# Optimization experiments

Hardware: AMD Instinct MI355X
Metric: run time of the kernel (lower is better)

The kernel has to match this reference:

```python
import jax, jax.numpy as jnp
import numpy as np

D = 1024      # n_embd
F = 1024      # moe_inter_dim (ffn_hidden_size)
E = 8         # moe_num_experts
K = 2         # moe_top_k
B, T = 2, 2048


def setup_inputs() -> dict:
    key = jax.random.key(0)
    ks = jax.random.split(key, 7)
    std = 0.02
    x = jax.random.normal(ks[0], (B, T, D), dtype=jnp.float32)
    router_w = jax.random.normal(ks[1], (D, E), dtype=jnp.float32) * std
    w1 = jax.random.normal(ks[2], (E, D, F), dtype=jnp.float32) * std  # expert up proj
    w2 = jax.random.normal(ks[3], (E, F, D), dtype=jnp.float32) * std  # expert down proj
    shared_gate_up = jax.random.normal(ks[4], (D, 2 * F), dtype=jnp.float32) * std
    shared_down = jax.random.normal(ks[5], (F, D), dtype=jnp.float32) * std
    shared_gate_w = jax.random.normal(ks[6], (D, 1), dtype=jnp.float32) * std
    return {"x": x, "router_w": router_w, "w1": w1, "w2": w2,
            "shared_gate_up": shared_gate_up, "shared_down": shared_down,
            "shared_gate_w": shared_gate_w}


def _moe_forward(x, router_w, w1, w2, shared_gate_up, shared_down, shared_gate_w):
    b, t, d = x.shape
    xf = x.reshape(-1, d)                                   # [N, D]
    n = xf.shape[0]

    # --- router: softmax over experts, top-k scores used directly as combine weights ---
    logits = xf @ router_w                                  # [N, E]
    probs = jax.nn.softmax(logits, axis=-1)
    topw, topi = jax.lax.top_k(probs, K)                    # [N, K]
    combine = jnp.zeros((n, E), dtype=probs.dtype).at[
        jnp.arange(n)[:, None], topi].add(topw)             # [N, E] sparse combine weights

    # --- expert MLP: h = silu(x @ w1_e) @ w2_e, combined with routing weights ---
    h = jax.nn.silu(jnp.einsum('nd,edf->nef', xf, w1))      # [N, E, F]
    ye = jnp.einsum('nef,efd->ned', h, w2)                  # [N, E, D]
    routed = jnp.einsum('ne,ned->nd', combine, ye)          # [N, D]

    # --- shared expert SwiGLU, gated by sigmoid(x @ shared_gate_w) ---
    gu = xf @ shared_gate_up                                # [N, 2F]
    gate, up = gu[:, :F], gu[:, F:]
    shared = (jax.nn.silu(gate) * up) @ shared_down         # [N, D]
    shared = jax.nn.sigmoid(xf @ shared_gate_w) * shared

    return (routed + shared).reshape(b, t, d)


def reference(x, router_w, w1, w2, shared_gate_up, shared_down, shared_gate_w):
    return _moe_forward(x, router_w, w1, w2, shared_gate_up, shared_down, shared_gate_w)
```

## Files before the change

### kernel.cpp

```cpp
#include <hip/hip_runtime.h>
#include <math.h>

typedef __bf16 bf16_t;
typedef __bf16 bf16x8 __attribute__((ext_vector_type(8)));
typedef __bf16 bf16x4 __attribute__((ext_vector_type(4)));
typedef float f32x4 __attribute__((ext_vector_type(4)));

#define N_TOK 4096
#define DMODEL 1024
#define FFN 1024
#define NEXP 8
#define HIST_BLK 16

#define BM 128
#define BN 128
#define BK 32
#define LDK 32

__device__ __forceinline__ void gload16(const bf16_t* g, bf16_t* l) {
  __builtin_amdgcn_global_load_lds((const __attribute__((address_space(1))) void*)g,
                                   (__attribute__((address_space(3))) void*)l, 16, 0, 0);
}

__global__ void transpose_all_kernel(const float* __restrict__ w1, const float* __restrict__ w2,
                                     const float* __restrict__ sgu, const float* __restrict__ sdw,
                                     bf16_t* __restrict__ w1t, bf16_t* __restrict__ w2t,
                                     bf16_t* __restrict__ sgut, bf16_t* __restrict__ sdt) {
  __shared__ float tile[32][33];
  const int z = blockIdx.z;
  const float* in;
  bf16_t* out;
  int C = 1024;
  bool remap = false;
  if (z < 8) {
    in = w1 + (size_t)z * 1048576; out = w1t + (size_t)z * 1048576;
  } else if (z < 16) {
    in = w2 + (size_t)(z - 8) * 1048576; out = w2t + (size_t)(z - 8) * 1048576;
  } else if (z == 16) {
    in = sgu; out = sgut; C = 2048; remap = true;
  } else {
    in = sdw; out = sdt;
  }
  const int R = 1024;
  const int c0 = blockIdx.x * 32, r0 = blockIdx.y * 32;
  if (c0 >= C) return;
  const int tx = threadIdx.x, ty = threadIdx.y;
#pragma unroll
  for (int i = 0; i < 32; i += 8)
    tile[ty + i][tx] = in[(size_t)(r0 + ty + i) * C + (c0 + tx)];
  __syncthreads();
#pragma unroll
  for (int i = 0; i < 32; i += 8) {
    int c = c0 + ty + i;
    int oc = remap ? ((c < FFN) ? 2 * c : 2 * (c - FFN) + 1) : c;
    out[(size_t)oc * R + (r0 + tx)] = (bf16_t)tile[tx][ty + i];
  }
}

__global__ void router_kernel(const float* __restrict__ x, const float* __restrict__ rw,
                              const float* __restrict__ gw, bf16_t* __restrict__ xb,
                              int* __restrict__ topi, float* __restrict__ topw,
                              float* __restrict__ sig) {
  const int t = blockIdx.x;
  const int lane = threadIdx.x;
  const float* xr = x + (size_t)t * DMODEL;
  bf16_t* xbr = xb + (size_t)t * DMODEL;
  float acc[NEXP] = {0.f, 0.f, 0.f, 0.f, 0.f, 0.f, 0.f, 0.f};
  float accg = 0.f;
#pragma unroll
  for (int i = 0; i < 4; i++) {
    const int d = i * 256 + lane * 4;
    float4 xv = *reinterpret_cast<const float4*>(xr + d);
    bf16x4 o;
    o[0] = (bf16_t)xv.x; o[1] = (bf16_t)xv.y; o[2] = (bf16_t)xv.z; o[3] = (bf16_t)xv.w;
    *reinterpret_cast<bf16x4*>(xbr + d) = o;
    const float xs[4] = {xv.x, xv.y, xv.z, xv.w};
#pragma unroll
    for (int j = 0; j < 4; j++) {
      const float4* r = reinterpret_cast<const float4*>(rw + (size_t)(d + j) * NEXP);
      float4 r0 = r[0], r1 = r[1];
      float xj = xs[j];
      acc[0] += xj * r0.x; acc[1] += xj * r0.y; acc[2] += xj * r0.z; acc[3] += xj * r0.w;
      acc[4] += xj * r1.x; acc[5] += xj * r1.y; acc[6] += xj * r1.z; acc[7] += xj * r1.w;
      accg += xj * gw[d + j];
    }
  }
#pragma unroll
  for (int e = 0; e < NEXP; e++)
    for (int s = 32; s > 0; s >>= 1) acc[e] += __shfl_down(acc[e], s, 64);
  for (int s = 32; s > 0; s >>= 1) accg += __shfl_down(accg, s, 64);
  if (lane == 0) {
    float mx = acc[0];
#pragma unroll
    for (int e = 1; e < NEXP; e++) mx = fmaxf(mx, acc[e]);
    float p[NEXP], sum = 0.f;
#pragma unroll
    for (int e = 0; e < NEXP; e++) { p[e] = __expf(acc[e] - mx); sum += p[e]; }
    int i1 = 0;
#pragma unroll
    for (int e = 1; e < NEXP; e++) if (acc[e] > acc[i1]) i1 = e;
    int i2 = (i1 == 0) ? 1 : 0;
#pragma unroll
    for (int e = 0; e < NEXP; e++) if (e != i1 && acc[e] > acc[i2]) i2 = e;
    float inv = 1.f / sum;
    topi[2 * t] = i1;     topw[2 * t] = p[i1] * inv;
    topi[2 * t + 1] = i2; topw[2 * t + 1] = p[i2] * inv;
    sig[t] = 1.f / (1.f + __expf(-accg));
  }
}

__global__ void hist_kernel(const int* __restrict__ topi, int* __restrict__ block_counts) {
  __shared__ int h[NEXP];
  const int tid = threadIdx.x;
  if (tid < NEXP) h[tid] = 0;
  __syncthreads();
  const int t = blockIdx.x * 256 + tid;
  atomicAdd(&h[topi[2 * t]], 1);
  atomicAdd(&h[topi[2 * t + 1]], 1);
  __syncthreads();
  if (tid < NEXP) block_counts[blockIdx.x * NEXP + tid] = h[tid];
}

__global__ void gather_kernel(const int* __restrict__ topi, const float* __restrict__ topw,
                              const int* __restrict__ block_counts, int* __restrict__ slot_tok,
                              float* __restrict__ slot_w, int* __restrict__ slot_of,
                              int* __restrict__ offsets, int* __restrict__ counts) {
  __shared__ int cur[NEXP];
  const int tid = threadIdx.x;
  if (tid < NEXP) {
    int off = 0;
    for (int f = 0; f < tid; f++)
      for (int b = 0; b < HIST_BLK; b++) off += block_counts[b * NEXP + f];
    int bb = off;
    for (int b = 0; b < (int)blockIdx.x; b++) bb += block_counts[b * NEXP + tid];
    cur[tid] = bb;
    if (blockIdx.x == 0) {
      offsets[tid] = off;
      int tot = 0;
      for (int b = 0; b < HIST_BLK; b++) tot += block_counts[b * NEXP + tid];
      counts[tid] = tot;
    }
  }
  __syncthreads();
  const int t = blockIdx.x * 256 + tid;
#pragma unroll
  for (int j = 0; j < 2; j++) {
    int e = topi[2 * t + j];
    int s = atomicAdd(&cur[e], 1);
    slot_tok[s] = t;
    slot_w[s] = topw[2 * t + j];
    slot_of[2 * t + j] = s;
  }
}

__global__ void combine_kernel(const bf16_t* __restrict__ Y, const int* __restrict__ slot_of,
                               float* __restrict__ out) {
  int i = blockIdx.x * blockDim.x + threadIdx.x;
  int t = i >> 7;
  int d = (i & 127) << 3;
  int s0 = slot_of[2 * t], s1 = slot_of[2 * t + 1];
  bf16x8 a = *reinterpret_cast<const bf16x8*>(Y + (size_t)s0 * DMODEL + d);
  bf16x8 b = *reinterpret_cast<const bf16x8*>(Y + (size_t)s1 * DMODEL + d);
  float* o = out + (size_t)t * DMODEL + d;
  float4 o0 = *reinterpret_cast<float4*>(o);
  float4 o1 = *reinterpret_cast<float4*>(o + 4);
  o0.x += (float)a[0] + (float)b[0]; o0.y += (float)a[1] + (float)b[1];
  o0.z += (float)a[2] + (float)b[2]; o0.w += (float)a[3] + (float)b[3];
  o1.x += (float)a[4] + (float)b[4]; o1.y += (float)a[5] + (float)b[5];
  o1.z += (float)a[6] + (float)b[6]; o1.w += (float)a[7] + (float)b[7];
  *reinterpret_cast<float4*>(o) = o0;
  *reinterpret_cast<float4*>(o + 4) = o1;
}

template <int MODE>
__global__ __launch_bounds__(256) void gemm_kernel(
    const bf16_t* __restrict__ A, const bf16_t* __restrict__ B, void* __restrict__ Cout,
    int N, const int* __restrict__ offsets, const int* __restrict__ counts,
    const int* __restrict__ slot_tok, const float* __restrict__ slot_w,
    const float* __restrict__ sig) {
  __shared__ bf16_t lds_a0[BM * LDK];
  __shared__ bf16_t lds_b0[BN * LDK];
  __shared__ bf16_t lds_a1[BM * LDK];
  __shared__ bf16_t lds_b1[BN * LDK];

  int bx_l, by_l, e_l;
  {
    const int bx = blockIdx.x, by = blockIdx.y, bz = blockIdx.z;
    if (MODE == 0) {
      const int f = by * 16 + bx;
      const int k = f & 7, s = f >> 3;
      by_l = k * 4 + (s & 3); bx_l = s >> 2; e_l = 0;
    } else if (MODE == 3) {
      const int f = by * 8 + bx;
      const int k = f & 7, s = f >> 3;
      by_l = k * 4 + (s & 3); bx_l = s >> 2; e_l = 0;
    } else {
      const int f = (bz * 32 + by) * 8 + bx;
      e_l = f & 7;
      const int s = f >> 3;
      by_l = s & 31; bx_l = s >> 5;
    }
  }

  const int e = e_l;
  int m0, mEnd;
  const bf16_t* Bp = B;
  if (MODE == 1 || MODE == 2) {
    const int off = offsets[e], cnt = counts[e];
    m0 = off + by_l * BM;
    mEnd = off + cnt;
    if (m0 >= mEnd) return;
    Bp += (size_t)e * FFN * DMODEL;
  } else {
    m0 = by_l * BM;
    mEnd = N_TOK;
  }
  const int n0 = bx_l * BN;

  const int tid = threadIdx.x;
  const int lane = tid & 63;
  const int wave = tid >> 6;
  const int wm = (wave >> 1) * 64;
  const int wn = (wave & 1) * 64;
  const int qd = lane >> 4;
  const int lm = lane & 15;

  const int srow = wave * 16 + (lane >> 2);
  const int chunk = (lane & 3) ^ ((lane >> 3) & 3);
  const bf16_t* pa[2];
  const bf16_t* pb[2];
#pragma unroll
  for (int h = 0; h < 2; h++) {
    int s = m0 + srow + h * 64;
    int sc = (s < mEnd) ? s : (mEnd - 1);
    int g;
    if (MODE == 1) g = slot_tok[sc];
    else if (MODE == 2) g = sc;
    else g = s;
    pa[h] = A + (size_t)g * 1024 + chunk * 8;
    pb[h] = Bp + (size_t)(n0 + srow + h * 64) * 1024 + chunk * 8;
  }

  f32x4 acc[4][4] = {};
  const int rkey = (lm >> 1) & 3;

#define STAGE(AB, BB, T)                                       \
  do {                                                         \
    const int k0s = (T) * BK;                                  \
    gload16(pa[0] + k0s, &AB[(wave * 16) * LDK]);              \
    gload16(pa[1] + k0s, &AB[(64 + wave * 16) * LDK]);         \
    gload16(pb[0] + k0s, &BB[(wave * 16) * LDK]);              \
    gload16(pb[1] + k0s, &BB[(64 + wave * 16) * LDK]);         \
  } while (0)

#define COMPUTE(AB, BB)                                                      \
  do {                                                                       \
    bf16x8 af[4], bfr[4];                                                    \
    _Pragma("unroll") for (int i = 0; i < 4; i++)                            \
        af[i] = *reinterpret_cast<const bf16x8*>(                            \
            &AB[(wm + i * 16 + lm) * LDK + ((qd ^ rkey) * 8)]);              \
    _Pragma("unroll") for (int j = 0; j < 4; j++)                            \
        bfr[j] = *reinterpret_cast<const bf16x8*>(                           \
            &BB[(wn + j * 16 + lm) * LDK + ((qd ^ rkey) * 8)]);              \
    _Pragma("unroll") for (int i = 0; i < 4; i++)                            \
        _Pragma("unroll") for (int j = 0; j < 4; j++)                        \
            acc[i][j] = __builtin_amdgcn_mfma_f32_16x16x32_bf16(             \
                af[i], bfr[j], acc[i][j], 0, 0, 0);                          \
  } while (0)

  STAGE(lds_a0, lds_b0, 0);
  __syncthreads();
  for (int t = 0; t < 32; t += 2) {
    STAGE(lds_a1, lds_b1, t + 1);
    COMPUTE(lds_a0, lds_b0);
    __syncthreads();
    if (t + 2 < 32) STAGE(lds_a0, lds_b0, t + 2);
    COMPUTE(lds_a1, lds_b1);
    __syncthreads();
  }
#undef COMPUTE
#undef STAGE

#pragma unroll
  for (int i = 0; i < 4; i++) {
#pragma unroll
    for (int r = 0; r < 4; r++) {
      const int gm = m0 + wm + i * 16 + qd * 4 + r;
      const bool mOk = (MODE == 0 || MODE == 3) || (gm < mEnd);
      const float wgt = (MODE == 2 && mOk) ? slot_w[gm] : 0.f;
#pragma unroll
      for (int j = 0; j < 4; j++) {
        const int col = n0 + wn + j * 16 + lm;
        float v = acc[i][j][r];
        if (MODE == 0) {
          float u = __shfl_xor(v, 1, 64);
          if ((lane & 1) == 0) {
            float sv = v / (1.f + __expf(-v)) * u;
            ((bf16_t*)Cout)[(size_t)gm * FFN + (col >> 1)] = (bf16_t)sv;
          }
        } else if (MODE == 1) {
          if (mOk) ((bf16_t*)Cout)[(size_t)gm * FFN + col] = (bf16_t)(v / (1.f + __expf(-v)));
        } else if (MODE == 2) {
          if (mOk) ((bf16_t*)Cout)[(size_t)gm * DMODEL + col] = (bf16_t)(wgt * v);
        } else {
          ((float*)Cout)[(size_t)gm * DMODEL + col] = sig[gm] * v;
        }
      }
    }
  }
}

extern "C" void kernel_launch(void* const* d_in, const int* in_sizes, int n_in, void* d_out,
                              int out_size, void* d_ws, size_t ws_size, hipStream_t stream) {
  const float* x = (const float*)d_in[0];
  const float* rw = (const float*)d_in[1];
  const float* w1 = (const float*)d_in[2];
  const float* w2 = (const float*)d_in[3];
  const float* sgu = (const float*)d_in[4];
  const float* sdw = (const float*)d_in[5];
  const float* gw = (const float*)d_in[6];
  float* out = (float*)d_out;

  char* ws = (char*)d_ws;
  size_t off = 0;
  auto alloc = [&](size_t bytes) -> void* {
    void* p = ws + off;
    off += (bytes + 255) & ~(size_t)255;
    return p;
  };
  bf16_t* xb = (bf16_t*)alloc((size_t)N_TOK * DMODEL * 2);
  bf16_t* w1t = (bf16_t*)alloc((size_t)NEXP * DMODEL * FFN * 2);
  bf16_t* w2t = (bf16_t*)alloc((size_t)NEXP * DMODEL * FFN * 2);
  bf16_t* sgut = (bf16_t*)alloc((size_t)2 * FFN * DMODEL * 2);
  bf16_t* sdt = (bf16_t*)alloc((size_t)DMODEL * FFN * 2);
  bf16_t* S = (bf16_t*)alloc((size_t)N_TOK * FFN * 2);
  bf16_t* H = (bf16_t*)alloc((size_t)N_TOK * 2 * FFN * 2);
  bf16_t* Y = (bf16_t*)alloc((size_t)N_TOK * 2 * DMODEL * 2);
  int* topi = (int*)alloc(N_TOK * 2 * 4);
  float* topw = (float*)alloc(N_TOK * 2 * 4);
  float* sig = (float*)alloc(N_TOK * 4);
  int* slot_tok = (int*)alloc(N_TOK * 2 * 4);
  float* slot_w = (float*)alloc(N_TOK * 2 * 4);
  int* slot_of = (int*)alloc(N_TOK * 2 * 4);
  int* block_counts = (int*)alloc(HIST_BLK * NEXP * 4);
  int* counts = (int*)alloc(NEXP * 4);
  int* offsets = (int*)alloc(NEXP * 4);

  transpose_all_kernel<<<dim3(64, 32, 18), dim3(32, 8), 0, stream>>>(w1, w2, sgu, sdw, w1t, w2t,
                                                                     sgut, sdt);
  router_kernel<<<N_TOK, 64, 0, stream>>>(x, rw, gw, xb, topi, topw, sig);
  hist_kernel<<<HIST_BLK, 256, 0, stream>>>(topi, block_counts);
  gather_kernel<<<HIST_BLK, 256, 0, stream>>>(topi, topw, block_counts, slot_tok, slot_w,
                                              slot_of, offsets, counts);

  gemm_kernel<0><<<dim3(2 * FFN / BN, N_TOK / BM, 1), 256, 0, stream>>>(
      xb, sgut, S, 2 * FFN, nullptr, nullptr, nullptr, nullptr, nullptr);
  gemm_kernel<1><<<dim3(FFN / BN, N_TOK / BM, NEXP), 256, 0, stream>>>(
      xb, w1t, H, FFN, offsets, counts, slot_tok, nullptr, nullptr);
  gemm_kernel<2><<<dim3(DMODEL / BN, N_TOK / BM, NEXP), 256, 0, stream>>>(
      H, w2t, Y, DMODEL, offsets, counts, slot_tok, slot_w, nullptr);
  gemm_kernel<3><<<dim3(DMODEL / BN, N_TOK / BM, 1), 256, 0, stream>>>(
      S, sdt, out, DMODEL, nullptr, nullptr, nullptr, nullptr, sig);
  combine_kernel<<<N_TOK * DMODEL / 8 / 256, 256, 0, stream>>>(Y, slot_of, out);
}
```

Baseline: 277.9 us.

## Fuse expert combine into down-proj GEMM via atomics; widen weight transpose tiles

The down-projection GEMM now scatters weighted results straight into the fp32 output with atomicAdd per element, keyed by slot token. This removes the bf16 Y buffer, the slot_of bookkeeping and the separate combine kernel, and it reorders launches so the shared-expert GEMM writes the output first. The weight transpose kernel also moves to 64x64 tiles with float4 loads and bf16x4 stores to cut memory transactions. The price is one fp32 atomic per output element, two per token, which contend and make the summation order nondeterministic.

```diff
diff --git a/kernel.cpp b/kernel.cpp
--- a/kernel.cpp
+++ b/kernel.cpp
@@ -26,7 +26,7 @@
                                      const float* __restrict__ sgu, const float* __restrict__ sdw,
                                      bf16_t* __restrict__ w1t, bf16_t* __restrict__ w2t,
                                      bf16_t* __restrict__ sgut, bf16_t* __restrict__ sdt) {
-  __shared__ float tile[32][33];
+  __shared__ float tile[64][65];
   const int z = blockIdx.z;
   const float* in;
   bf16_t* out;
@@ -42,18 +42,31 @@
     in = sdw; out = sdt;
   }
   const int R = 1024;
-  const int c0 = blockIdx.x * 32, r0 = blockIdx.y * 32;
+  const int c0 = blockIdx.x * 64, r0 = blockIdx.y * 64;
   if (c0 >= C) return;
-  const int tx = threadIdx.x, ty = threadIdx.y;
-#pragma unroll
-  for (int i = 0; i < 32; i += 8)
-    tile[ty + i][tx] = in[(size_t)(r0 + ty + i) * C + (c0 + tx)];
-  __syncthreads();
-#pragma unroll
-  for (int i = 0; i < 32; i += 8) {
-    int c = c0 + ty + i;
-    int oc = remap ? ((c < FFN) ? 2 * c : 2 * (c - FFN) + 1) : c;
-    out[(size_t)oc * R + (r0 + tx)] = (bf16_t)tile[tx][ty + i];
+  const int tid = threadIdx.x;
+  const int cf = tid & 15;
+  const int rr = tid >> 4;
+#pragma unroll
+  for (int p = 0; p < 4; p++) {
+    const int row = rr + p * 16;
+    float4 v = *reinterpret_cast<const float4*>(in + (size_t)(r0 + row) * C + c0 + cf * 4);
+    tile[row][cf * 4 + 0] = v.x;
+    tile[row][cf * 4 + 1] = v.y;
+    tile[row][cf * 4 + 2] = v.z;
+    tile[row][cf * 4 + 3] = v.w;
+  }
+  __syncthreads();
+  const int r4 = (tid & 15) * 4;
+  const int ocl = tid >> 4;
+#pragma unroll
+  for (int p = 0; p < 4; p++) {
+    const int c = c0 + ocl + p * 16;
+    const int oc = remap ? ((c < FFN) ? 2 * c : 2 * (c - FFN) + 1) : c;
+    bf16x4 o;
+#pragma unroll
+    for (int j = 0; j < 4; j++) o[j] = (bf16_t)tile[r4 + j][ocl + p * 16];
+    *reinterpret_cast<bf16x4*>(out + (size_t)oc * R + r0 + r4) = o;
   }
 }
 
@@ -123,7 +136,7 @@
 
 __global__ void gather_kernel(const int* __restrict__ topi, const float* __restrict__ topw,
                               const int* __restrict__ block_counts, int* __restrict__ slot_tok,
-                              float* __restrict__ slot_w, int* __restrict__ slot_of,
+                              float* __restrict__ slot_w,
                               int* __restrict__ offsets, int* __restrict__ counts) {
   __shared__ int cur[NEXP];
   const int tid = threadIdx.x;
@@ -149,27 +162,7 @@
     int s = atomicAdd(&cur[e], 1);
     slot_tok[s] = t;
     slot_w[s] = topw[2 * t + j];
-    slot_of[2 * t + j] = s;
-  }
-}
-
-__global__ void combine_kernel(const bf16_t* __restrict__ Y, const int* __restrict__ slot_of,
-                               float* __restrict__ out) {
-  int i = blockIdx.x * blockDim.x + threadIdx.x;
-  int t = i >> 7;
-  int d = (i & 127) << 3;
-  int s0 = slot_of[2 * t], s1 = slot_of[2 * t + 1];
-  bf16x8 a = *reinterpret_cast<const bf16x8*>(Y + (size_t)s0 * DMODEL + d);
-  bf16x8 b = *reinterpret_cast<const bf16x8*>(Y + (size_t)s1 * DMODEL + d);
-  float* o = out + (size_t)t * DMODEL + d;
-  float4 o0 = *reinterpret_cast<float4*>(o);
-  float4 o1 = *reinterpret_cast<float4*>(o + 4);
-  o0.x += (float)a[0] + (float)b[0]; o0.y += (float)a[1] + (float)b[1];
-  o0.z += (float)a[2] + (float)b[2]; o0.w += (float)a[3] + (float)b[3];
-  o1.x += (float)a[4] + (float)b[4]; o1.y += (float)a[5] + (float)b[5];
-  o1.z += (float)a[6] + (float)b[6]; o1.w += (float)a[7] + (float)b[7];
-  *reinterpret_cast<float4*>(o) = o0;
-  *reinterpret_cast<float4*>(o + 4) = o1;
+  }
 }
 
 template <int MODE>
@@ -288,6 +281,7 @@
       const int gm = m0 + wm + i * 16 + qd * 4 + r;
       const bool mOk = (MODE == 0 || MODE == 3) || (gm < mEnd);
       const float wgt = (MODE == 2 && mOk) ? slot_w[gm] : 0.f;
+      const int tok = (MODE == 2 && mOk) ? slot_tok[gm] : 0;
 #pragma unroll
       for (int j = 0; j < 4; j++) {
         const int col = n0 + wn + j * 16 + lm;
@@ -301,7 +295,7 @@
         } else if (MODE == 1) {
           if (mOk) ((bf16_t*)Cout)[(size_t)gm * FFN + col] = (bf16_t)(v / (1.f + __expf(-v)));
         } else if (MODE == 2) {
-          if (mOk) ((bf16_t*)Cout)[(size_t)gm * DMODEL + col] = (bf16_t)(wgt * v);
+          if (mOk) atomicAdd(&((float*)Cout)[(size_t)tok * DMODEL + col], wgt * v);
         } else {
           ((float*)Cout)[(size_t)gm * DMODEL + col] = sig[gm] * v;
         }
@@ -335,31 +329,28 @@
   bf16_t* sdt = (bf16_t*)alloc((size_t)DMODEL * FFN * 2);
   bf16_t* S = (bf16_t*)alloc((size_t)N_TOK * FFN * 2);
   bf16_t* H = (bf16_t*)alloc((size_t)N_TOK * 2 * FFN * 2);
-  bf16_t* Y = (bf16_t*)alloc((size_t)N_TOK * 2 * DMODEL * 2);
   int* topi = (int*)alloc(N_TOK * 2 * 4);
   float* topw = (float*)alloc(N_TOK * 2 * 4);
   float* sig = (float*)alloc(N_TOK * 4);
   int* slot_tok = (int*)alloc(N_TOK * 2 * 4);
   float* slot_w = (float*)alloc(N_TOK * 2 * 4);
-  int* slot_of = (int*)alloc(N_TOK * 2 * 4);
   int* block_counts = (int*)alloc(HIST_BLK * NEXP * 4);
   int* counts = (int*)alloc(NEXP * 4);
   int* offsets = (int*)alloc(NEXP * 4);
 
-  transpose_all_kernel<<<dim3(64, 32, 18), dim3(32, 8), 0, stream>>>(w1, w2, sgu, sdw, w1t, w2t,
-                                                                     sgut, sdt);
+  transpose_all_kernel<<<dim3(32, 16, 18), 256, 0, stream>>>(w1, w2, sgu, sdw, w1t, w2t,
+                                                             sgut, sdt);
   router_kernel<<<N_TOK, 64, 0, stream>>>(x, rw, gw, xb, topi, topw, sig);
   hist_kernel<<<HIST_BLK, 256, 0, stream>>>(topi, block_counts);
   gather_kernel<<<HIST_BLK, 256, 0, stream>>>(topi, topw, block_counts, slot_tok, slot_w,
-                                              slot_of, offsets, counts);
+                                              offsets, counts);
 
   gemm_kernel<0><<<dim3(2 * FFN / BN, N_TOK / BM, 1), 256, 0, stream>>>(
       xb, sgut, S, 2 * FFN, nullptr, nullptr, nullptr, nullptr, nullptr);
   gemm_kernel<1><<<dim3(FFN / BN, N_TOK / BM, NEXP), 256, 0, stream>>>(
       xb, w1t, H, FFN, offsets, counts, slot_tok, nullptr, nullptr);
-  gemm_kernel<2><<<dim3(DMODEL / BN, N_TOK / BM, NEXP), 256, 0, stream>>>(
-      H, w2t, Y, DMODEL, offsets, counts, slot_tok, slot_w, nullptr);
   gemm_kernel<3><<<dim3(DMODEL / BN, N_TOK / BM, 1), 256, 0, stream>>>(
       S, sdt, out, DMODEL, nullptr, nullptr, nullptr, nullptr, sig);
-  combine_kernel<<<N_TOK * DMODEL / 8 / 256, 256, 0, stream>>>(Y, slot_of, out);
-}
+  gemm_kernel<2><<<dim3(DMODEL / BN, N_TOK / BM, NEXP), 256, 0, stream>>>(
+      H, w2t, out, DMODEL, offsets, counts, slot_tok, slot_w, nullptr);
+}
```

Result: slower. 288.4 us (+3.8%).
